# Optimization experiments

Hardware: AMD Instinct MI355X
Metric: run time of the kernel (lower is better)

The kernel has to match this reference:

```python
import jax, jax.numpy as jnp
import numpy as np

D_MODEL = 1024
NUM_HEADS = 16
D_K = D_MODEL // NUM_HEADS
FFN_SIZE = 4096
EPS = 1e-6


def _layer_norm(x, gamma, beta):
    mu = jnp.mean(x, axis=-1, keepdims=True)
    var = jnp.var(x, axis=-1, keepdims=True)
    return (x - mu) / jnp.sqrt(var + EPS) * gamma + beta


def setup_inputs() -> dict:
    key = jax.random.key(0)
    ks = jax.random.split(key, 12)
    B, S = 2, 2048
    s_attn = 1.0 / np.sqrt(D_MODEL)
    s_ffn1 = 1.0 / np.sqrt(D_MODEL)
    s_ffn2 = 1.0 / np.sqrt(FFN_SIZE)
    return {
        "x": jax.random.normal(ks[0], (B, S, D_MODEL), dtype=jnp.float32),
        "W_q": jax.random.normal(ks[1], (D_MODEL, D_MODEL), dtype=jnp.float32) * s_attn,
        "W_k": jax.random.normal(ks[2], (D_MODEL, D_MODEL), dtype=jnp.float32) * s_attn,
        "W_v": jax.random.normal(ks[3], (D_MODEL, D_MODEL), dtype=jnp.float32) * s_attn,
        "W_o": jax.random.normal(ks[4], (D_MODEL, D_MODEL), dtype=jnp.float32) * s_attn,
        "b_o": jnp.zeros((D_MODEL,), dtype=jnp.float32),
        "W1": jax.random.normal(ks[5], (D_MODEL, FFN_SIZE), dtype=jnp.float32) * s_ffn1,
        "b1": jnp.zeros((FFN_SIZE,), dtype=jnp.float32),
        "W2": jax.random.normal(ks[6], (FFN_SIZE, D_MODEL), dtype=jnp.float32) * s_ffn2,
        "b2": jnp.zeros((D_MODEL,), dtype=jnp.float32),
        "ln1_g": jnp.ones((D_MODEL,), dtype=jnp.float32),
        "ln1_b": jnp.zeros((D_MODEL,), dtype=jnp.float32),
        "ln2_g": jnp.ones((D_MODEL,), dtype=jnp.float32),
        "ln2_b": jnp.zeros((D_MODEL,), dtype=jnp.float32),
    }


def reference(x, W_q, W_k, W_v, W_o, b_o, W1, b1, W2, b2,
              ln1_g, ln1_b, ln2_g, ln2_b):
    B, S, _ = x.shape

    # --- self-attention sublayer (pre-norm residual) ---
    h = _layer_norm(x, ln1_g, ln1_b)
    q = (h @ W_q).reshape(B, S, NUM_HEADS, D_K).transpose(0, 2, 1, 3)  # [B,H,S,Dk]
    k = (h @ W_k).reshape(B, S, NUM_HEADS, D_K).transpose(0, 2, 1, 3)
    v = (h @ W_v).reshape(B, S, NUM_HEADS, D_K).transpose(0, 2, 1, 3)
    scores = jnp.einsum("bhqd,bhkd->bhqk", q, k) / jnp.sqrt(jnp.float32(D_K))
    attn = jax.nn.softmax(scores, axis=-1)
    ctx = jnp.einsum("bhqk,bhkd->bhqd", attn, v)
    ctx = ctx.transpose(0, 2, 1, 3).reshape(B, S, D_MODEL)
    x = x + (ctx @ W_o + b_o)

    # --- FFN sublayer (pre-norm residual) ---
    h2 = _layer_norm(x, ln2_g, ln2_b)
    f = jax.nn.relu(h2 @ W1 + b1) @ W2 + b2
    return x + f
```

## Files before the change

### kernel.cpp

```cpp
#include <hip/hip_runtime.h>
#include <cstdint>
#include <cstddef>


typedef __attribute__((ext_vector_type(8))) __bf16 bf16x8;
typedef __attribute__((ext_vector_type(4))) __bf16 bf16x4;
typedef __attribute__((ext_vector_type(4))) float f32x4;

__device__ __forceinline__ void async16(const void* g, void* l) {
  __builtin_amdgcn_global_load_lds(
      (__attribute__((address_space(1))) void*)g,
      (__attribute__((address_space(3))) void*)l, 16, 0, 0);
}

__device__ __forceinline__ f32x4 mfma16(bf16x8 a, bf16x8 b, f32x4 c) {
  return __builtin_amdgcn_mfma_f32_16x16x32_bf16(a, b, c, 0, 0, 0);
}

__global__ __launch_bounds__(256) void transpose_all(
    const float* __restrict__ Wq, const float* __restrict__ Wk,
    const float* __restrict__ Wv, const float* __restrict__ Wo,
    const float* __restrict__ W1, const float* __restrict__ W2,
    __bf16* __restrict__ WqkvT, __bf16* __restrict__ WoT,
    __bf16* __restrict__ W1T, __bf16* __restrict__ W2T) {
  const int id = blockIdx.x;
  const float* in;
  __bf16* out;
  int ld_in, ld_out, c0, r0;
  if (id < 1024) {
    const int which = id >> 8, tl = id & 255;
    c0 = (tl & 15) * 64;
    r0 = (tl >> 4) * 64;
    ld_in = 1024;
    ld_out = 1024;
    if (which == 0) { in = Wq; out = WqkvT; }
    else if (which == 1) { in = Wk; out = WqkvT + 1048576; }
    else if (which == 2) { in = Wv; out = WqkvT + 2097152; }
    else { in = Wo; out = WoT; }
  } else if (id < 2048) {
    const int tl = id - 1024;
    c0 = (tl & 63) * 64;
    r0 = (tl >> 6) * 64;
    in = W1; out = W1T; ld_in = 4096; ld_out = 1024;
  } else {
    const int tl = id - 2048;
    c0 = (tl & 15) * 64;
    r0 = (tl >> 4) * 64;
    in = W2; out = W2T; ld_in = 1024; ld_out = 4096;
  }
  __shared__ __bf16 tile[64][65];
  const int tx = threadIdx.x & 63, ty = threadIdx.x >> 6;
#pragma unroll
  for (int i = 0; i < 16; i++) {
    int r = ty + i * 4;
    tile[r][tx] = (__bf16)in[(size_t)(r0 + r) * ld_in + c0 + tx];
  }
  __syncthreads();
#pragma unroll
  for (int i = 0; i < 16; i++) {
    int r = ty + i * 4;
    out[(size_t)(c0 + r) * ld_out + r0 + tx] = tile[tx][r];
  }
}

__global__ __launch_bounds__(256) void transpose_bf16(
    const unsigned short* __restrict__ in, unsigned short* __restrict__ out,
    int ld_in, int ld_out) {
  __shared__ unsigned short tile[64][65];
  const int c0 = blockIdx.x * 64, r0 = blockIdx.y * 64;
  const int tx = threadIdx.x & 63, ty = threadIdx.x >> 6;
#pragma unroll
  for (int i = 0; i < 16; i++) {
    int r = ty + i * 4;
    tile[r][tx] = in[(size_t)(r0 + r) * ld_in + c0 + tx];
  }
  __syncthreads();
#pragma unroll
  for (int i = 0; i < 16; i++) {
    int r = ty + i * 4;
    out[(size_t)(c0 + r) * ld_out + r0 + tx] = tile[tx][r];
  }
}

__global__ __launch_bounds__(256) void ln_kernel(
    const float* __restrict__ xin, const float* __restrict__ g,
    const float* __restrict__ bt, __bf16* __restrict__ out) {
  const int tok = blockIdx.x * 4 + (threadIdx.x >> 6);
  const int lane = threadIdx.x & 63;
  const int base0 = lane * 8, base1 = 512 + lane * 8;
  const float* xr = xin + (size_t)tok * 1024;
  float v[16];
  float4 a0 = *(const float4*)(xr + base0);
  float4 a1 = *(const float4*)(xr + base0 + 4);
  float4 a2 = *(const float4*)(xr + base1);
  float4 a3 = *(const float4*)(xr + base1 + 4);
  v[0] = a0.x; v[1] = a0.y; v[2] = a0.z; v[3] = a0.w;
  v[4] = a1.x; v[5] = a1.y; v[6] = a1.z; v[7] = a1.w;
  v[8] = a2.x; v[9] = a2.y; v[10] = a2.z; v[11] = a2.w;
  v[12] = a3.x; v[13] = a3.y; v[14] = a3.z; v[15] = a3.w;
  float s = 0.f, s2 = 0.f;
#pragma unroll
  for (int i = 0; i < 16; i++) { s += v[i]; s2 += v[i] * v[i]; }
#pragma unroll
  for (int m = 1; m < 64; m <<= 1) {
    s += __shfl_xor(s, m);
    s2 += __shfl_xor(s2, m);
  }
  const float mean = s * (1.f / 1024.f);
  const float var = s2 * (1.f / 1024.f) - mean * mean;
  const float rstd = rsqrtf(var + 1e-6f);
  float4 g0 = *(const float4*)(g + base0), g1 = *(const float4*)(g + base0 + 4);
  float4 g2 = *(const float4*)(g + base1), g3 = *(const float4*)(g + base1 + 4);
  float4 b0 = *(const float4*)(bt + base0), b1v = *(const float4*)(bt + base0 + 4);
  float4 b2v = *(const float4*)(bt + base1), b3 = *(const float4*)(bt + base1 + 4);
  float gg[16] = {g0.x, g0.y, g0.z, g0.w, g1.x, g1.y, g1.z, g1.w,
                  g2.x, g2.y, g2.z, g2.w, g3.x, g3.y, g3.z, g3.w};
  float bb[16] = {b0.x, b0.y, b0.z, b0.w, b1v.x, b1v.y, b1v.z, b1v.w,
                  b2v.x, b2v.y, b2v.z, b2v.w, b3.x, b3.y, b3.z, b3.w};
  bf16x8 o0, o1;
#pragma unroll
  for (int j = 0; j < 8; j++) {
    o0[j] = (__bf16)((v[j] - mean) * rstd * gg[j] + bb[j]);
    o1[j] = (__bf16)((v[8 + j] - mean) * rstd * gg[8 + j] + bb[8 + j]);
  }
  __bf16* op = out + (size_t)tok * 1024;
  *(bf16x8*)(op + base0) = o0;
  *(bf16x8*)(op + base1) = o1;
}

template <int EPI, int TM, int SPLITS = 1>
__global__ __launch_bounds__(256) void gemm_bt(
    const __bf16* __restrict__ A, int lda, const __bf16* __restrict__ BT,
    int ldb, void* __restrict__ C, int ldc, int Kb,
    const float* __restrict__ bias, const float* __restrict__ res, int ldres) {
  const int t = threadIdx.x;
  const int m0 = blockIdx.x * TM, n0 = blockIdx.y * 128;
  const int kz = (SPLITS > 1) ? blockIdx.z : 0;
  __shared__ __align__(16) __bf16 As[2][TM * 32];
  __shared__ __align__(16) __bf16 Bs[2][128 * 32];
  const int lane = t & 63, w = t >> 6;
  const int quad = lane >> 4, l15 = lane & 15;
  const int wm = w >> 1, wn = w & 1;
  constexpr int MF = TM / 32;

  f32x4 acc[MF][4] = {};

  const int swc = ((t & 3) ^ ((t >> 3) & 3)) * 8;
  const __bf16* ga = A + (size_t)(m0 + (t >> 2)) * lda + swc + (size_t)kz * Kb;
  const __bf16* gb = BT + (size_t)(n0 + (t >> 2)) * ldb + swc + (size_t)kz * Kb;
  const size_t a64 = (size_t)64 * lda, b64 = (size_t)64 * ldb;

  auto stage = [&](int buf) {
#pragma unroll
    for (int i = 0; i < TM / 64; i++)
      async16(ga + i * a64, As[buf] + t * 8 + i * 2048);
    async16(gb, Bs[buf] + t * 8);
    async16(gb + b64, Bs[buf] + t * 8 + 2048);
  };
  const int ce = (quad ^ ((l15 >> 1) & 3)) * 8;
  auto compute = [&](int buf) {
    bf16x8 af[MF], bfr[4];
#pragma unroll
    for (int i = 0; i < MF; i++)
      af[i] = *(const bf16x8*)&As[buf][(wm * (TM / 2) + i * 16 + l15) * 32 + ce];
#pragma unroll
    for (int i = 0; i < 4; i++)
      bfr[i] = *(const bf16x8*)&Bs[buf][(wn * 64 + i * 16 + l15) * 32 + ce];
#pragma unroll
    for (int mi = 0; mi < MF; mi++)
#pragma unroll
      for (int ni = 0; ni < 4; ni++)
        acc[mi][ni] = mfma16(af[mi], bfr[ni], acc[mi][ni]);
  };

  stage(0);
  ga += 32;
  gb += 32;
  __syncthreads();
  int cur = 0;
  const int iters = Kb / 32;
  for (int it = 0; it < iters - 1; ++it) {
    stage(cur ^ 1);
    ga += 32;
    gb += 32;
    compute(cur);
    __syncthreads();
    cur ^= 1;
  }
  compute(cur);

  float biasv[4];
  if constexpr (EPI != 0) {
#pragma unroll
    for (int ni = 0; ni < 4; ni++)
      biasv[ni] = bias[n0 + wn * 64 + ni * 16 + l15];
  }
  __bf16* Cb = (__bf16*)C;
  if constexpr (SPLITS > 1)
    Cb += (size_t)kz * gridDim.x * TM * ldc;
#pragma unroll
  for (int mi = 0; mi < MF; mi++)
#pragma unroll
    for (int ni = 0; ni < 4; ni++)
#pragma unroll
      for (int r = 0; r < 4; r++) {
        const int row = m0 + wm * (TM / 2) + mi * 16 + quad * 4 + r;
        const int col = n0 + wn * 64 + ni * 16 + l15;
        float v = acc[mi][ni][r];
        if constexpr (EPI == 0) {
          Cb[(size_t)row * ldc + col] = (__bf16)v;
        } else if constexpr (EPI == 1) {
          v += biasv[ni] + res[(size_t)row * ldres + col];
          ((float*)C)[(size_t)row * ldc + col] = v;
        } else {
          v += biasv[ni];
          ((__bf16*)C)[(size_t)row * ldc + col] = (__bf16)fmaxf(v, 0.f);
        }
      }
}

__global__ __launch_bounds__(256) void reduce_split(
    const __bf16* __restrict__ P, const float* __restrict__ bias,
    const float* __restrict__ res, float* __restrict__ out) {
  const int row = blockIdx.x, c = threadIdx.x * 4;
  const size_t i = (size_t)row * 1024 + c;
  bf16x4 p0 = *(const bf16x4*)(P + i);
  bf16x4 p1 = *(const bf16x4*)(P + 4194304 + i);
  float4 r = *(const float4*)(res + i);
  float4 bv = *(const float4*)(bias + c);
  float4 o;
  o.x = (float)p0[0] + (float)p1[0] + r.x + bv.x;
  o.y = (float)p0[1] + (float)p1[1] + r.y + bv.y;
  o.z = (float)p0[2] + (float)p1[2] + r.z + bv.z;
  o.w = (float)p0[3] + (float)p1[3] + r.w + bv.w;
  *(float4*)(out + i) = o;
}

__global__ __launch_bounds__(256, 4) void attn_kernel(
    const __bf16* __restrict__ QKV, const __bf16* __restrict__ VT,
    __bf16* __restrict__ ctx) {
  const int qt = blockIdx.x, bh = blockIdx.y;
  const int b = bh >> 4, h = bh & 15;
  const int t = threadIdx.x, w = t >> 6, lane = t & 63;
  const int quad = lane >> 4, l15 = lane & 15;
  const int tok0 = b * 2048;
  const int q0w = tok0 + qt * 64 + w * 16;

  __shared__ __align__(16) __bf16 Ks[128 * 64];
  __shared__ __align__(16) __bf16 VTs[64 * 128];

  const float qs = 0.18033688011112042f;
  bf16x8 qf[2];
#pragma unroll
  for (int kb = 0; kb < 2; kb++) {
    const __bf16* src =
        QKV + (size_t)(q0w + l15) * 3072 + h * 64 + kb * 32 + quad * 8;
    bf16x8 r = *(const bf16x8*)src;
#pragma unroll
    for (int j = 0; j < 8; j++) r[j] = (__bf16)((float)r[j] * qs);
    qf[kb] = r;
  }

  f32x4 lacc = {};
  f32x4 O[4] = {};

  const int krow = t >> 3;
  const int kcg = (((t & 7) ^ (krow & 7)) * 8);
  const int vrow = t >> 4;
  const int vcg = (((2 * (t & 15)) ^ ((vrow & 7) * 2)) * 4);
  const int sub = 4 * (quad & 1);
  const int qh = quad >> 1;

  for (int kt = 0; kt < 16; ++kt) {
    const int ktok = tok0 + kt * 128;
#pragma unroll
    for (int j = 0; j < 4; j++) {
      const __bf16* gp =
          QKV + (size_t)(ktok + krow + j * 32) * 3072 + 1024 + h * 64 + kcg;
      async16(gp, Ks + t * 8 + j * 2048);
    }
#pragma unroll
    for (int j = 0; j < 4; j++) {
      const __bf16* gp =
          VT + (size_t)(h * 64 + vrow + j * 16) * 4096 + ktok + vcg;
      async16(gp, VTs + t * 8 + j * 2048);
    }
    __syncthreads();

    f32x4 sT[8];
#pragma unroll
    for (int kt8 = 0; kt8 < 8; kt8++) {
      f32x4 a = {};
#pragma unroll
      for (int kb = 0; kb < 2; kb++) {
        bf16x8 kf = *(const bf16x8*)&Ks[(kt8 * 16 + l15) * 64 +
                                        (((kb * 4 + quad) ^ (l15 & 7)) * 8)];
        a = mfma16(kf, qf[kb], a);
      }
      sT[kt8] = a;
    }

    bf16x8 pf[4];
#pragma unroll
    for (int kb = 0; kb < 4; kb++)
#pragma unroll
      for (int hf = 0; hf < 2; hf++)
#pragma unroll
        for (int r = 0; r < 4; r++) {
          const float p = __builtin_amdgcn_exp2f(sT[2 * kb + hf][r]);
          lacc[r] += p;
          pf[kb][hf * 4 + r] = (__bf16)p;
        }

#pragma unroll
    for (int kb = 0; kb < 4; kb++) {
      const int g0 = (((4 * kb + qh) ^ (l15 & 7)) * 8) + sub;
      const int g1 = (((4 * kb + 2 + qh) ^ (l15 & 7)) * 8) + sub;
#pragma unroll
      for (int nd = 0; nd < 4; nd++) {
        const int base = (nd * 16 + l15) * 128;
        bf16x4 a0 = *(const bf16x4*)&VTs[base + g0];
        bf16x4 a1 = *(const bf16x4*)&VTs[base + g1];
        bf16x8 vf;
        vf[0] = a0[0]; vf[1] = a0[1]; vf[2] = a0[2]; vf[3] = a0[3];
        vf[4] = a1[0]; vf[5] = a1[1]; vf[6] = a1[2]; vf[7] = a1[3];
        O[nd] = mfma16(pf[kb], vf, O[nd]);
      }
    }
    __syncthreads();
  }

  float lsum = lacc[0] + lacc[1] + lacc[2] + lacc[3];
  lsum += __shfl_xor(lsum, 16);
  lsum += __shfl_xor(lsum, 32);
  float rl[4];
#pragma unroll
  for (int r = 0; r < 4; r++) rl[r] = 1.0f / __shfl(lsum, quad * 4 + r);
#pragma unroll
  for (int nd = 0; nd < 4; nd++)
#pragma unroll
    for (int r = 0; r < 4; r++) {
      const int tokq = q0w + quad * 4 + r;
      const int col = h * 64 + nd * 16 + l15;
      ctx[(size_t)tokq * 1024 + col] = (__bf16)(O[nd][r] * rl[r]);
    }
}

extern "C" void kernel_launch(void* const* d_in, const int* in_sizes, int n_in,
                              void* d_out, int out_size, void* d_ws,
                              size_t ws_size, hipStream_t stream) {
  (void)in_sizes; (void)n_in; (void)out_size; (void)ws_size;

  const float* x = (const float*)d_in[0];
  const float* Wq = (const float*)d_in[1];
  const float* Wk = (const float*)d_in[2];
  const float* Wv = (const float*)d_in[3];
  const float* Wo = (const float*)d_in[4];
  const float* b_o = (const float*)d_in[5];
  const float* W1 = (const float*)d_in[6];
  const float* b1 = (const float*)d_in[7];
  const float* W2 = (const float*)d_in[8];
  const float* b2 = (const float*)d_in[9];
  const float* ln1g = (const float*)d_in[10];
  const float* ln1b = (const float*)d_in[11];
  const float* ln2g = (const float*)d_in[12];
  const float* ln2b = (const float*)d_in[13];

  char* ws = (char*)d_ws;
  __bf16* WqkvT = (__bf16*)(ws + 0);
  __bf16* WoT = (__bf16*)(ws + 6291456);
  __bf16* W1T = (__bf16*)(ws + 8388608);
  __bf16* W2T = (__bf16*)(ws + 16777216);
  __bf16* h = (__bf16*)(ws + 25165824);
  __bf16* QKV = (__bf16*)(ws + 33554432);
  __bf16* VT = (__bf16*)(ws + 58720256);
  __bf16* ctx = (__bf16*)(ws + 67108864);
  float* x1 = (float*)(ws + 75497472);
  __bf16* f1 = QKV;
  __bf16* Pw2 = (__bf16*)(ws + 0);

  const dim3 blk(256);

  transpose_all<<<dim3(3072), blk, 0, stream>>>(Wq, Wk, Wv, Wo, W1, W2, WqkvT,
                                                WoT, W1T, W2T);

  ln_kernel<<<dim3(1024), blk, 0, stream>>>(x, ln1g, ln1b, h);

  gemm_bt<0, 128><<<dim3(32, 24), blk, 0, stream>>>(
      h, 1024, WqkvT, 1024, (void*)QKV, 3072, 1024, nullptr, nullptr, 0);

  transpose_bf16<<<dim3(16, 64), blk, 0, stream>>>(
      (const unsigned short*)(QKV + 2048), (unsigned short*)VT, 3072, 4096);

  attn_kernel<<<dim3(32, 32), blk, 0, stream>>>(QKV, VT, ctx);

  gemm_bt<1, 64><<<dim3(64, 8), blk, 0, stream>>>(
      ctx, 1024, WoT, 1024, (void*)x1, 1024, 1024, b_o, x, 1024);

  ln_kernel<<<dim3(1024), blk, 0, stream>>>(x1, ln2g, ln2b, h);

  gemm_bt<2, 128><<<dim3(32, 32), blk, 0, stream>>>(
      h, 1024, W1T, 1024, (void*)f1, 4096, 1024, b1, nullptr, 0);

  gemm_bt<0, 128, 2><<<dim3(32, 8, 2), blk, 0, stream>>>(
      f1, 4096, W2T, 4096, (void*)Pw2, 1024, 2048, nullptr, nullptr, 0);
  reduce_split<<<dim3(4096), blk, 0, stream>>>(Pw2, b2, x1, (float*)d_out);
}
```

Measured before the change: 357.1 us.

## Triple-buffer GEMM LDS staging with explicit vmcnt waits and raw barriers

The bf16 GEMM main loop goes from double to triple LDS buffering, so loads run two k-steps ahead of compute. Each step now waits with a targeted `s_waitcnt vmcnt(N)` and a raw `s_barrier` instead of `__syncthreads`, which drains all outstanding memory operations. The aim is to hide more global-load latency and avoid full waits on each iteration. In exchange, LDS use per block grows by half, which may lower occupancy, and the hand-written wait counts must match the number of loads issued per stage.

```diff
diff --git a/kernel.cpp b/kernel.cpp
--- a/kernel.cpp
+++ b/kernel.cpp
@@ -15,6 +15,20 @@
 
 __device__ __forceinline__ f32x4 mfma16(bf16x8 a, bf16x8 b, f32x4 c) {
   return __builtin_amdgcn_mfma_f32_16x16x32_bf16(a, b, c, 0, 0, 0);
+}
+
+template <int N>
+__device__ __forceinline__ void wait_vmcnt() {
+  if constexpr (N == 0) {
+    asm volatile("s_waitcnt vmcnt(0)" ::: "memory");
+  } else if constexpr (N == 3) {
+    asm volatile("s_waitcnt vmcnt(3)" ::: "memory");
+  } else {
+    asm volatile("s_waitcnt vmcnt(4)" ::: "memory");
+  }
+}
+__device__ __forceinline__ void barrier_raw() {
+  asm volatile("s_barrier" ::: "memory");
 }
 
 __global__ __launch_bounds__(256) void transpose_all(
@@ -136,12 +150,13 @@
   const int t = threadIdx.x;
   const int m0 = blockIdx.x * TM, n0 = blockIdx.y * 128;
   const int kz = (SPLITS > 1) ? blockIdx.z : 0;
-  __shared__ __align__(16) __bf16 As[2][TM * 32];
-  __shared__ __align__(16) __bf16 Bs[2][128 * 32];
+  __shared__ __align__(16) __bf16 As[3][TM * 32];
+  __shared__ __align__(16) __bf16 Bs[3][128 * 32];
   const int lane = t & 63, w = t >> 6;
   const int quad = lane >> 4, l15 = lane & 15;
   const int wm = w >> 1, wn = w & 1;
   constexpr int MF = TM / 32;
+  constexpr int LOADS = TM / 64 + 2;
 
   f32x4 acc[MF][4] = {};
 
@@ -156,6 +171,8 @@
       async16(ga + i * a64, As[buf] + t * 8 + i * 2048);
     async16(gb, Bs[buf] + t * 8);
     async16(gb + b64, Bs[buf] + t * 8 + 2048);
+    ga += 32;
+    gb += 32;
   };
   const int ce = (quad ^ ((l15 >> 1) & 3)) * 8;
   auto compute = [&](int buf) {
@@ -173,20 +190,20 @@
         acc[mi][ni] = mfma16(af[mi], bfr[ni], acc[mi][ni]);
   };
 
+  const int iters = Kb / 32;
   stage(0);
-  ga += 32;
-  gb += 32;
-  __syncthreads();
-  int cur = 0;
-  const int iters = Kb / 32;
+  stage(1);
+  int cur = 0, stg = 2;
   for (int it = 0; it < iters - 1; ++it) {
-    stage(cur ^ 1);
-    ga += 32;
-    gb += 32;
+    wait_vmcnt<LOADS>();
+    barrier_raw();
+    if (it + 2 < iters) stage(stg);
     compute(cur);
-    __syncthreads();
-    cur ^= 1;
-  }
+    cur = (cur == 2) ? 0 : cur + 1;
+    stg = (stg == 2) ? 0 : stg + 1;
+  }
+  wait_vmcnt<0>();
+  barrier_raw();
   compute(cur);
 
   float biasv[4];
```

New measurement: 347.0 us. -2.8%, faster.
